# Optimization experiments

Hardware: AMD Instinct MI355X
Metric: run time of the kernel (lower is better)

Reference implementation:

```python
import jax, jax.numpy as jnp
import numpy as np

DIM = 512
MAX_LEN = 2048
SHARED = 128
EXPAND = 2 * DIM  # expansion_factor * dim
PROJ = 2 * EXPAND + SHARED
EPS = 1e-6
BATCH = 8


def _rope(x):
    # x: [n, d]; rotates last dim (split-half RoPE) with position along axis 0
    n, d = x.shape
    half = d // 2
    freq = jnp.arange(half, dtype=x.dtype) / float(half)
    inv_freq = 10000.0 ** (-freq)
    sinusoid = jnp.arange(n, dtype=x.dtype)[:, None] * inv_freq[None, :]  # [n, half]
    sin, cos = jnp.sin(sinusoid), jnp.cos(sinusoid)
    x1, x2 = x[:, :half], x[:, half:]
    return jnp.concatenate([x1 * cos - x2 * sin, x2 * cos + x1 * sin], axis=-1)


def _toeplitz_rope(n, a, b):
    # a, b: [max_len]; tile to [n, max_len], rope over positions, then outer product
    ar = _rope(jnp.tile(a[None, :], (n, 1)))
    br = _rope(jnp.tile(b[None, :], (n, 1)))
    return jnp.einsum('mk,nk->mn', ar, br)  # [n, n]


def setup_inputs() -> dict:
    key = jax.random.key(0)
    ks = jax.random.split(key, 8)
    std = 0.02
    return {
        'x': jax.random.normal(ks[0], (BATCH, MAX_LEN, DIM), jnp.float32),
        'W1': std * jax.random.normal(ks[1], (DIM, PROJ), jnp.float32),
        'b1': jnp.zeros((PROJ,), jnp.float32),
        'W2': std * jax.random.normal(ks[2], (EXPAND, DIM), jnp.float32),
        'b2': jnp.zeros((DIM,), jnp.float32),
        'rope_a': std * jax.random.normal(ks[3], (MAX_LEN,), jnp.float32),
        'rope_b': std * jax.random.normal(ks[4], (MAX_LEN,), jnp.float32),
        'gamma': std * jax.random.normal(ks[5], (2, SHARED), jnp.float32),
        'beta': jnp.zeros((2, SHARED), jnp.float32),
        'norm_scale': jnp.asarray(1.0, jnp.float32),
    }


def reference(x, W1, b1, W2, b2, rope_a, rope_b, gamma, beta, norm_scale):
    shortcut = x
    # ScaledNorm: x * rsqrt(mean(x^2)) * scale
    ms = jnp.mean(jnp.square(x), axis=-1, keepdims=True)
    xn = x * jax.lax.rsqrt(ms + EPS) * norm_scale
    # proj1 with swish activation
    uv = jax.nn.swish(xn @ W1 + b1)  # [b, n, PROJ]
    u = uv[..., :EXPAND]
    v = uv[..., EXPAND:2 * EXPAND]
    base = uv[..., 2 * EXPAND:]  # [b, n, SHARED]
    qk_base = base[:, :, None, :] * gamma + beta  # [b, n, 2, SHARED]
    q, k = qk_base[:, :, 0, :], qk_base[:, :, 1, :]
    qk = jnp.einsum('bnd,bmd->bnm', q, k) / float(MAX_LEN)
    qk = qk + _toeplitz_rope(MAX_LEN, rope_a, rope_b)
    kernel = jnp.square(jax.nn.relu(qk))  # sqrrelu
    o = u * jnp.einsum('bnm,bme->bne', kernel, v)
    return o @ W2 + b2 + shortcut
```

## Files before the change

### kernel.cpp

```cpp
#include <hip/hip_runtime.h>
#include <math.h>

#define SEQ    2048
#define DIMM   512
#define SH     128
#define EXP    1024
#define PROJ_  2176
#define NBATCH 8
#define ROWS   16384

#define KER_SCALE     16384.0f
#define KER_SCALE_INV (1.0f / 16384.0f)
#define QK_INV        (1.0f / (4096.0f * 2048.0f))
#define W8            64.0f
#define INV4096       (1.0f / 4096.0f)

typedef __attribute__((ext_vector_type(4))) float floatx4;
typedef __attribute__((ext_vector_type(8))) int   int8v;

__device__ __forceinline__ unsigned short f2bf(float f) {
  union { float f; unsigned int u; } v; v.f = f;
  unsigned int r = (v.u + 0x7fffu + ((v.u >> 16) & 1u)) >> 16;
  return (unsigned short)r;
}
__device__ __forceinline__ float bf2f(unsigned short h) {
  union { unsigned int u; float f; } v; v.u = ((unsigned int)h) << 16;
  return v.f;
}
__device__ __forceinline__ unsigned char f2fp8(float f) {
  return (unsigned char)(__builtin_amdgcn_cvt_pk_fp8_f32(f, 0.0f, 0, false) & 0xffu);
}
__device__ __forceinline__ unsigned int pk4fp8(float a, float b, float c, float d) {
  unsigned int w = __builtin_amdgcn_cvt_pk_fp8_f32(a, b, 0, false);
  return __builtin_amdgcn_cvt_pk_fp8_f32(c, d, w, true);
}
__device__ __forceinline__ float fp82f(unsigned char b) {
  int e = (b >> 3) & 15, m = b & 7;
  float v = ldexpf((float)(e ? (8 + m) : m), (e ? e : 1) - 10);
  return (b & 0x80) ? -v : v;
}

#if defined(__has_builtin)
#if __has_builtin(__builtin_amdgcn_cvt_f32_fp8)
#define HAVE_HW_FP8DEC 1
#endif
#endif
#ifdef HAVE_HW_FP8DEC
#define FP8DEC0(w) __builtin_amdgcn_cvt_f32_fp8((w), 0)
#define FP8DEC1(w) __builtin_amdgcn_cvt_f32_fp8((w), 1)
#define FP8DEC2(w) __builtin_amdgcn_cvt_f32_fp8((w), 2)
#define FP8DEC3(w) __builtin_amdgcn_cvt_f32_fp8((w), 3)
#else
#define FP8DEC0(w) fp82f((unsigned char)((w)))
#define FP8DEC1(w) fp82f((unsigned char)((w) >> 8))
#define FP8DEC2(w) fp82f((unsigned char)((w) >> 16))
#define FP8DEC3(w) fp82f((unsigned char)((w) >> 24))
#endif

__device__ __forceinline__ void async16(const void* g, void* l) {
  __builtin_amdgcn_global_load_lds(
      (const __attribute__((address_space(1))) void*)g,
      (__attribute__((address_space(3))) void*)l, 16, 0, 0);
}

__device__ __forceinline__ void transpose_tile_fp8(const float* __restrict__ in,
                                                   unsigned char* __restrict__ out,
                                                   int R, int C, int bx, int by, float* tile) {
  int tx = threadIdx.x & 31, ty = threadIdx.x >> 5;
  int c0 = bx * 32, r0 = by * 32;
  #pragma unroll
  for (int j = 0; j < 32; j += 8)
    tile[(ty + j) * 33 + tx] = in[(long)(r0 + ty + j) * C + c0 + tx];
  __syncthreads();
  #pragma unroll
  for (int j = 0; j < 32; j += 8)
    out[(long)(c0 + ty + j) * R + r0 + tx] = f2fp8(tile[tx * 33 + ty + j] * W8);
}

__global__ void prep_kernel(const float* __restrict__ x, const float* __restrict__ ns,
                            unsigned char* __restrict__ xq,
                            const float* __restrict__ W1, unsigned char* __restrict__ w1q,
                            const float* __restrict__ W2, unsigned char* __restrict__ w2q,
                            const float* __restrict__ ra, const float* __restrict__ rb,
                            float* __restrict__ tpl) {
  __shared__ float sh[33 * 32];
  const int b = blockIdx.x, tid = threadIdx.x;
  if (b < 4096) {
    int wave = tid >> 6, lane = tid & 63;
    long row = (long)b * 4 + wave;
    const float4* xr = (const float4*)(x + row * DIMM);
    float4 v0 = xr[lane], v1 = xr[lane + 64];
    float ss = v0.x*v0.x + v0.y*v0.y + v0.z*v0.z + v0.w*v0.w
             + v1.x*v1.x + v1.y*v1.y + v1.z*v1.z + v1.w*v1.w;
    #pragma unroll
    for (int o = 32; o > 0; o >>= 1) ss += __shfl_xor(ss, o);
    float sc = rsqrtf(ss * (1.0f / DIMM) + 1e-6f) * ns[0] * W8;
    uint2 pk;
    pk.x = pk4fp8(v0.x*sc, v0.y*sc, v0.z*sc, v0.w*sc);
    pk.y = pk4fp8(v1.x*sc, v1.y*sc, v1.z*sc, v1.w*sc);
    ((uint2*)(xq + row * DIMM))[lane] = pk;
  } else if (b < 6144) {
    const int d = b - 4096;
    float sc_ = 0.0f, ss_ = 0.0f;
    for (int k = tid; k < 1024; k += 256) {
      float a1 = ra[k], a2 = ra[k + 1024];
      float b1v = rb[k], b2v = rb[k + 1024];
      float p = a1 * b1v + a2 * b2v;
      float q = a1 * b2v - a2 * b1v;
      float th = exp2f((float)k * (-13.287712379549449f / 1024.0f));
      float ang = (float)d * th;
      sc_ += p * cosf(ang);
      ss_ += q * sinf(ang);
    }
    #pragma unroll
    for (int o = 32; o > 0; o >>= 1) {
      sc_ += __shfl_xor(sc_, o);
      ss_ += __shfl_xor(ss_, o);
    }
    int wave = tid >> 6, lane = tid & 63;
    if (lane == 0) { sh[wave] = sc_; sh[8 + wave] = ss_; }
    __syncthreads();
    if (tid == 0) {
      float Sc = sh[0] + sh[1] + sh[2] + sh[3];
      float Ss = sh[8] + sh[9] + sh[10] + sh[11];
      tpl[2047 + d] = Sc + Ss;
      if (d > 0) tpl[2047 - d] = Sc - Ss;
    }
  } else if (b < 7232) {
    int t = b - 6144;
    transpose_tile_fp8(W1, w1q, DIMM, PROJ_, t % 68, t / 68, sh);
  } else {
    int t = b - 7232;
    transpose_tile_fp8(W2, w2q, EXP, DIMM, t % 16, t / 16, sh);
  }
}

__device__ __forceinline__ void mfma_core_mx(const unsigned char* __restrict__ A,
                                             const unsigned char* __restrict__ B,
                                             int K, long rowBase, long colBase,
                                             unsigned char* smem, floatx4 acc[4][4]) {
  const int tid  = threadIdx.x;
  const int wave = tid >> 6;
  const int lane = tid & 63;
  const int wr   = (wave >> 1) * 64;
  const int wc   = (wave & 1) * 64;
  const int r_l  = lane >> 3;
  const int c8   = lane & 7;
  const int fm   = lane & 15;
  const int fq   = lane >> 4;

  floatx4 z = {0.0f, 0.0f, 0.0f, 0.0f};
  #pragma unroll
  for (int mi = 0; mi < 4; ++mi)
    #pragma unroll
    for (int ni = 0; ni < 4; ++ni) acc[mi][ni] = z;

  const unsigned char* aSrc[4];
  const unsigned char* bSrc[4];
  int ldsOff[4];
  #pragma unroll
  for (int j = 0; j < 4; ++j) {
    int row = j * 32 + wave * 8 + r_l;
    int g = c8 ^ (row & 7);
    aSrc[j] = A + (rowBase + row) * (long)K + g * 16;
    bSrc[j] = B + (colBase + row) * (long)K + g * 16;
    ldsOff[j] = (j * 32 + wave * 8) * 128;
  }

  union U8 { uint4 q[2]; int8v v; };
  const int nt = K >> 7;

  #pragma unroll
  for (int j = 0; j < 4; ++j) {
    async16(aSrc[j], smem + ldsOff[j]);
    async16(bSrc[j], smem + 16384 + ldsOff[j]);
  }
  if (nt > 1) {
    #pragma unroll
    for (int j = 0; j < 4; ++j) {
      async16(aSrc[j] + 128, smem + 32768 + ldsOff[j]);
      async16(bSrc[j] + 128, smem + 49152 + ldsOff[j]);
    }
  }

  int cur = 0;
  for (int t = 0; t < nt; ++t) {
    if (t + 1 < nt) {
      asm volatile("s_waitcnt vmcnt(8)" ::: "memory");
    } else {
      asm volatile("s_waitcnt vmcnt(0)" ::: "memory");
    }
    __builtin_amdgcn_s_barrier();
    __builtin_amdgcn_sched_barrier(0);

    const unsigned char* As = smem + cur * 32768;
    const unsigned char* Bs = As + 16384;
    int8v av[4], bv[4];
    #pragma unroll
    for (int mi = 0; mi < 4; ++mi) {
      int row = wr + mi * 16 + fm;
      int s0 = (2 * fq) ^ (row & 7);
      U8 u;
      u.q[0] = *(const uint4*)(As + row * 128 + s0 * 16);
      u.q[1] = *(const uint4*)(As + row * 128 + (s0 ^ 1) * 16);
      av[mi] = u.v;
    }
    #pragma unroll
    for (int ni = 0; ni < 4; ++ni) {
      int row = wc + ni * 16 + fm;
      int s0 = (2 * fq) ^ (row & 7);
      U8 u;
      u.q[0] = *(const uint4*)(Bs + row * 128 + s0 * 16);
      u.q[1] = *(const uint4*)(Bs + row * 128 + (s0 ^ 1) * 16);
      bv[ni] = u.v;
    }
    if (t + 2 < nt) {
      asm volatile("s_waitcnt lgkmcnt(0)" ::: "memory");
      __builtin_amdgcn_sched_barrier(0);
      __builtin_amdgcn_s_barrier();
      unsigned char* nb = smem + cur * 32768;
      int k0 = (t + 2) << 7;
      #pragma unroll
      for (int j = 0; j < 4; ++j) {
        async16(aSrc[j] + k0, nb + ldsOff[j]);
        async16(bSrc[j] + k0, nb + 16384 + ldsOff[j]);
      }
    }

    __builtin_amdgcn_s_setprio(1);
    #pragma unroll
    for (int mi = 0; mi < 4; ++mi)
      #pragma unroll
      for (int ni = 0; ni < 4; ++ni)
        acc[mi][ni] = __builtin_amdgcn_mfma_scale_f32_16x16x128_f8f6f4(
            av[mi], bv[ni], acc[mi][ni], 0, 0, 0, 0x7F7F7F7F, 0, 0x7F7F7F7F);
    __builtin_amdgcn_s_setprio(0);
    cur ^= 1;
  }
}

#define EPILOGUE_VARS                                         \
  const int lane = threadIdx.x & 63, wave = threadIdx.x >> 6; \
  const int wr = (wave >> 1) * 64, wc = (wave & 1) * 64;      \
  const int fr = (lane >> 4) * 4, fc = lane & 15;

__global__ void __launch_bounds__(256)
gemm_uv(const unsigned char* __restrict__ xq,
        const unsigned char* __restrict__ w1q,
        const float* __restrict__ b1,
        const float* __restrict__ gamma,
        const float* __restrict__ beta,
        unsigned char* __restrict__ uq,
        unsigned char* __restrict__ vT,
        unsigned char* __restrict__ qq,
        unsigned char* __restrict__ kq) {
  __shared__ __align__(16) unsigned char smem8[65536];
  floatx4 acc[4][4];
  long rowBase = (long)blockIdx.x * 128;
  long colBase = (long)blockIdx.y * 128;
  mfma_core_mx(xq, w1q, DIMM, rowBase, colBase, smem8, acc);
  EPILOGUE_VARS

  if (blockIdx.y < 8) {
    #pragma unroll
    for (int ni = 0; ni < 4; ++ni) {
      long col = colBase + wc + ni * 16 + fc;
      float bb = b1[col];
      #pragma unroll
      for (int mi = 0; mi < 4; ++mi)
      #pragma unroll
      for (int i = 0; i < 4; ++i) {
        long row = rowBase + wr + mi * 16 + fr + i;
        float t = acc[mi][ni][i] * INV4096 + bb;
        uq[row * EXP + col] = f2fp8(t / (1.0f + __expf(-t)) * W8);
      }
    }
  } else if (blockIdx.y < 16) {
    __syncthreads();
    #pragma unroll
    for (int ni = 0; ni < 4; ++ni) {
      int cl = wc + ni * 16 + fc;
      float bb = b1[colBase + cl];
      #pragma unroll
      for (int mi = 0; mi < 4; ++mi) {
        int rl = wr + mi * 16 + fr;
        float v[4];
        #pragma unroll
        for (int i = 0; i < 4; ++i) {
          float t = acc[mi][ni][i] * INV4096 + bb;
          v[i] = t / (1.0f + __expf(-t));
        }
        *(unsigned int*)(smem8 + cl * 136 + rl) = pk4fp8(v[0], v[1], v[2], v[3]);
      }
    }
    __syncthreads();
    long b_   = rowBase >> 11;
    long nblk = rowBase & 2047;
    long e0   = colBase - EXP;
    #pragma unroll
    for (int rep = 0; rep < 4; ++rep) {
      int cl = rep * 32 + (threadIdx.x >> 3);
      int n0 = (threadIdx.x & 7) * 16;
      uint4 v16 = *(const uint4*)(smem8 + cl * 136 + n0);
      *(uint4*)(vT + (b_ * EXP + e0 + cl) * (long)SEQ + nblk + n0) = v16;
    }
  } else {
    #pragma unroll
    for (int ni = 0; ni < 4; ++ni) {
      long col = colBase + wc + ni * 16 + fc;
      int dd = (int)(col - 2 * EXP);
      float bb = b1[col];
      float g0 = gamma[dd], g1 = gamma[SH + dd];
      float be0 = beta[dd], be1 = beta[SH + dd];
      #pragma unroll
      for (int mi = 0; mi < 4; ++mi)
      #pragma unroll
      for (int i = 0; i < 4; ++i) {
        long row = rowBase + wr + mi * 16 + fr + i;
        float t = acc[mi][ni][i] * INV4096 + bb;
        float s = t / (1.0f + __expf(-t));
        qq[row * SH + dd] = f2fp8((s * g0 + be0) * W8);
        kq[row * SH + dd] = f2fp8((s * g1 + be1) * W8);
      }
    }
  }
}

__global__ void __launch_bounds__(256)
gemm_qk(const unsigned char* __restrict__ kq,
        const unsigned char* __restrict__ qq,
        const float* __restrict__ tpl,
        unsigned char* __restrict__ ker) {
  __shared__ __align__(16) unsigned char smem8[33792];
  float* tplS = (float*)(smem8 + 32768);
  floatx4 acc[4][4];
  int L = blockIdx.x;
  long b = L & 7;
  int w = L >> 3;
  long mBase = (long)(w & 15) * 128;
  long nBase = (long)(w >> 4) * 128;
  long D = nBase - mBase;
  if (threadIdx.x < 64)
    ((float4*)tplS)[threadIdx.x] = *(const float4*)(tpl + D + 1920 + 4 * (long)threadIdx.x);
  mfma_core_mx(kq + b * SEQ * SH, qq + b * SEQ * SH, SH, mBase, nBase, smem8, acc);
  unsigned char* kerb = ker + b * (long)SEQ * SEQ;
  EPILOGUE_VARS
  (void)fr;
  __syncthreads();
  #pragma unroll
  for (int mi = 0; mi < 4; ++mi)
  #pragma unroll
  for (int ni = 0; ni < 4; ++ni) {
    int m_loc0 = wr + mi * 16 + (lane >> 4) * 4;
    int n_loc  = wc + ni * 16 + fc;
    float v[4];
    #pragma unroll
    for (int i = 0; i < 4; ++i) {
      float val = acc[mi][ni][i] * QK_INV + tplS[n_loc - m_loc0 - i + 127];
      float r = fmaxf(val, 0.0f);
      v[i] = fminf(r * r * KER_SCALE, 440.0f);
    }
    *(unsigned int*)(smem8 + n_loc * 136 + m_loc0) = pk4fp8(v[0], v[1], v[2], v[3]);
  }
  __syncthreads();
  #pragma unroll
  for (int rep = 0; rep < 4; ++rep) {
    int n_loc = rep * 32 + (threadIdx.x >> 3);
    int m_seg = (threadIdx.x & 7) * 16;
    uint4 v16 = *(const uint4*)(smem8 + n_loc * 136 + m_seg);
    *(uint4*)(kerb + (nBase + n_loc) * (long)SEQ + mBase + m_seg) = v16;
  }
}

__global__ void __launch_bounds__(256)
gemm_pv(const unsigned char* __restrict__ ker,
        const unsigned char* __restrict__ vT,
        const unsigned char* __restrict__ uq,
        unsigned char* __restrict__ obq) {
  __shared__ __align__(16) unsigned char smem8[65536];
  floatx4 acc[4][4];
  int L = blockIdx.x;
  long b = L & 7;
  int w = L >> 3;
  long eBase = (long)(w & 7) * 128;
  long nBase = (long)(w >> 3) * 128;
  mfma_core_mx(vT + b * (long)EXP * SEQ, ker + b * (long)SEQ * SEQ, SEQ,
               eBase, nBase, smem8, acc);
  const unsigned char* ub = uq + b * (long)SEQ * EXP;
  unsigned char* obb = obq + b * (long)SEQ * EXP;
  EPILOGUE_VARS
  (void)fr;
  __syncthreads();
  #pragma unroll
  for (int mi = 0; mi < 4; ++mi)
  #pragma unroll
  for (int ni = 0; ni < 4; ++ni) {
    int e_loc0 = wr + mi * 16 + (lane >> 4) * 4;
    int n_loc  = wc + ni * 16 + fc;
    unsigned int uw = *(const unsigned int*)(ub + (nBase + n_loc) * (long)EXP + eBase + e_loc0);
    float u0 = FP8DEC0(uw), u1 = FP8DEC1(uw), u2 = FP8DEC2(uw), u3 = FP8DEC3(uw);
    float v0 = acc[mi][ni][0] * KER_SCALE_INV * u0;
    float v1 = acc[mi][ni][1] * KER_SCALE_INV * u1;
    float v2 = acc[mi][ni][2] * KER_SCALE_INV * u2;
    float v3 = acc[mi][ni][3] * KER_SCALE_INV * u3;
    *(unsigned int*)(smem8 + n_loc * 136 + e_loc0) = pk4fp8(v0, v1, v2, v3);
  }
  __syncthreads();
  #pragma unroll
  for (int rep = 0; rep < 4; ++rep) {
    int n_loc = rep * 32 + (threadIdx.x >> 3);
    int e_seg = (threadIdx.x & 7) * 16;
    uint4 v16 = *(const uint4*)(smem8 + n_loc * 136 + e_seg);
    *(uint4*)(obb + (nBase + n_loc) * (long)EXP + eBase + e_seg) = v16;
  }
}

__global__ void __launch_bounds__(256)
gemm_out(const unsigned char* __restrict__ obq,
         const unsigned char* __restrict__ w2q,
         const float* __restrict__ b2,
         const float* __restrict__ x,
         float* __restrict__ out) {
  __shared__ __align__(16) unsigned char smem8[65536];
  floatx4 acc[4][4];
  long rowBase = (long)blockIdx.x * 128;
  long colBase = (long)blockIdx.y * 128;
  mfma_core_mx(obq, w2q, EXP, rowBase, colBase, smem8, acc);
  EPILOGUE_VARS
  #pragma unroll
  for (int mi = 0; mi < 4; ++mi)
  #pragma unroll
  for (int ni = 0; ni < 4; ++ni)
  #pragma unroll
  for (int i = 0; i < 4; ++i) {
    long row = rowBase + wr + mi * 16 + fr + i;
    long col = colBase + wc + ni * 16 + fc;
    out[row * DIMM + col] = acc[mi][ni][i] * INV4096 + b2[col] + x[row * DIMM + col];
  }
}

extern "C" void kernel_launch(void* const* d_in, const int* in_sizes, int n_in,
                              void* d_out, int out_size, void* d_ws, size_t ws_size,
                              hipStream_t stream) {
  const float* x          = (const float*)d_in[0];
  const float* W1         = (const float*)d_in[1];
  const float* b1         = (const float*)d_in[2];
  const float* W2         = (const float*)d_in[3];
  const float* b2         = (const float*)d_in[4];
  const float* rope_a     = (const float*)d_in[5];
  const float* rope_b     = (const float*)d_in[6];
  const float* gamma      = (const float*)d_in[7];
  const float* beta       = (const float*)d_in[8];
  const float* norm_scale = (const float*)d_in[9];
  float* out = (float*)d_out;

  char* ws = (char*)d_ws;
  size_t off = 0;
  auto nxt = [&](size_t bytes) -> void* {
    void* p = ws + off;
    off += (bytes + 255) & ~(size_t)255;
    return p;
  };
  unsigned char*  xq  = (unsigned char*)nxt((size_t)ROWS * DIMM);
  unsigned char*  w1q = (unsigned char*)nxt((size_t)PROJ_ * DIMM);
  unsigned char*  w2q = (unsigned char*)nxt((size_t)DIMM * EXP);
  unsigned char*  uq  = (unsigned char*)nxt((size_t)ROWS * EXP);
  unsigned char*  vT  = (unsigned char*)nxt((size_t)NBATCH * EXP * SEQ);
  unsigned char*  qq  = (unsigned char*)nxt((size_t)ROWS * SH);
  unsigned char*  kq  = (unsigned char*)nxt((size_t)ROWS * SH);
  float*          tpl = (float*)nxt((size_t)4096 * 4);
  unsigned char*  ker = (unsigned char*)nxt((size_t)NBATCH * SEQ * SEQ);
  unsigned char*  obq = (unsigned char*)nxt((size_t)ROWS * EXP);

  prep_kernel<<<7744, 256, 0, stream>>>(x, norm_scale, xq, W1, w1q, W2, w2q,
                                        rope_a, rope_b, tpl);
  gemm_uv<<<dim3(ROWS / 128, PROJ_ / 128), 256, 0, stream>>>(xq, w1q, b1, gamma, beta,
                                                             uq, vT, qq, kq);
  gemm_qk<<<2048, 256, 0, stream>>>(kq, qq, tpl, ker);
  gemm_pv<<<1024, 256, 0, stream>>>(ker, vT, uq, obq);
  gemm_out<<<dim3(ROWS / 128, DIMM / 128), 256, 0, stream>>>(obq, w2q, b2, x, out);
}
```

Measured before the change: 209.9 us.

## Recompute u projection inside PV GEMM instead of materializing uq

```diff
diff --git a/kernel.cpp b/kernel.cpp
--- a/kernel.cpp
+++ b/kernel.cpp
@@ -39,23 +39,6 @@
   float v = ldexpf((float)(e ? (8 + m) : m), (e ? e : 1) - 10);
   return (b & 0x80) ? -v : v;
 }
-
-#if defined(__has_builtin)
-#if __has_builtin(__builtin_amdgcn_cvt_f32_fp8)
-#define HAVE_HW_FP8DEC 1
-#endif
-#endif
-#ifdef HAVE_HW_FP8DEC
-#define FP8DEC0(w) __builtin_amdgcn_cvt_f32_fp8((w), 0)
-#define FP8DEC1(w) __builtin_amdgcn_cvt_f32_fp8((w), 1)
-#define FP8DEC2(w) __builtin_amdgcn_cvt_f32_fp8((w), 2)
-#define FP8DEC3(w) __builtin_amdgcn_cvt_f32_fp8((w), 3)
-#else
-#define FP8DEC0(w) fp82f((unsigned char)((w)))
-#define FP8DEC1(w) fp82f((unsigned char)((w) >> 8))
-#define FP8DEC2(w) fp82f((unsigned char)((w) >> 16))
-#define FP8DEC3(w) fp82f((unsigned char)((w) >> 24))
-#endif
 
 __device__ __forceinline__ void async16(const void* g, void* l) {
   __builtin_amdgcn_global_load_lds(
@@ -250,32 +233,17 @@
         const float* __restrict__ b1,
         const float* __restrict__ gamma,
         const float* __restrict__ beta,
-        unsigned char* __restrict__ uq,
         unsigned char* __restrict__ vT,
         unsigned char* __restrict__ qq,
         unsigned char* __restrict__ kq) {
   __shared__ __align__(16) unsigned char smem8[65536];
   floatx4 acc[4][4];
   long rowBase = (long)blockIdx.x * 128;
-  long colBase = (long)blockIdx.y * 128;
+  long colBase = (long)(blockIdx.y + 8) * 128;
   mfma_core_mx(xq, w1q, DIMM, rowBase, colBase, smem8, acc);
   EPILOGUE_VARS
 
   if (blockIdx.y < 8) {
-    #pragma unroll
-    for (int ni = 0; ni < 4; ++ni) {
-      long col = colBase + wc + ni * 16 + fc;
-      float bb = b1[col];
-      #pragma unroll
-      for (int mi = 0; mi < 4; ++mi)
-      #pragma unroll
-      for (int i = 0; i < 4; ++i) {
-        long row = rowBase + wr + mi * 16 + fr + i;
-        float t = acc[mi][ni][i] * INV4096 + bb;
-        uq[row * EXP + col] = f2fp8(t / (1.0f + __expf(-t)) * W8);
-      }
-    }
-  } else if (blockIdx.y < 16) {
     __syncthreads();
     #pragma unroll
     for (int ni = 0; ni < 4; ++ni) {
@@ -375,35 +343,38 @@
 __global__ void __launch_bounds__(256)
 gemm_pv(const unsigned char* __restrict__ ker,
         const unsigned char* __restrict__ vT,
-        const unsigned char* __restrict__ uq,
+        const unsigned char* __restrict__ xq,
+        const unsigned char* __restrict__ w1q,
+        const float* __restrict__ b1,
         unsigned char* __restrict__ obq) {
   __shared__ __align__(16) unsigned char smem8[65536];
-  floatx4 acc[4][4];
+  floatx4 accU[4][4], accP[4][4];
   int L = blockIdx.x;
   long b = L & 7;
   int w = L >> 3;
   long eBase = (long)(w & 7) * 128;
   long nBase = (long)(w >> 3) * 128;
+  mfma_core_mx(w1q, xq + b * (long)SEQ * DIMM, DIMM, eBase, nBase, smem8, accU);
+  __syncthreads();
   mfma_core_mx(vT + b * (long)EXP * SEQ, ker + b * (long)SEQ * SEQ, SEQ,
-               eBase, nBase, smem8, acc);
-  const unsigned char* ub = uq + b * (long)SEQ * EXP;
+               eBase, nBase, smem8, accP);
   unsigned char* obb = obq + b * (long)SEQ * EXP;
   EPILOGUE_VARS
-  (void)fr;
   __syncthreads();
   #pragma unroll
   for (int mi = 0; mi < 4; ++mi)
   #pragma unroll
   for (int ni = 0; ni < 4; ++ni) {
-    int e_loc0 = wr + mi * 16 + (lane >> 4) * 4;
+    int e_loc0 = wr + mi * 16 + fr;
     int n_loc  = wc + ni * 16 + fc;
-    unsigned int uw = *(const unsigned int*)(ub + (nBase + n_loc) * (long)EXP + eBase + e_loc0);
-    float u0 = FP8DEC0(uw), u1 = FP8DEC1(uw), u2 = FP8DEC2(uw), u3 = FP8DEC3(uw);
-    float v0 = acc[mi][ni][0] * KER_SCALE_INV * u0;
-    float v1 = acc[mi][ni][1] * KER_SCALE_INV * u1;
-    float v2 = acc[mi][ni][2] * KER_SCALE_INV * u2;
-    float v3 = acc[mi][ni][3] * KER_SCALE_INV * u3;
-    *(unsigned int*)(smem8 + n_loc * 136 + e_loc0) = pk4fp8(v0, v1, v2, v3);
+    float v[4];
+    #pragma unroll
+    for (int i = 0; i < 4; ++i) {
+      float t = accU[mi][ni][i] * INV4096 + b1[eBase + e_loc0 + i];
+      float s = t / (1.0f + __expf(-t)) * W8;
+      v[i] = accP[mi][ni][i] * KER_SCALE_INV * s;
+    }
+    *(unsigned int*)(smem8 + n_loc * 136 + e_loc0) = pk4fp8(v[0], v[1], v[2], v[3]);
   }
   __syncthreads();
   #pragma unroll
@@ -464,7 +435,6 @@
   unsigned char*  xq  = (unsigned char*)nxt((size_t)ROWS * DIMM);
   unsigned char*  w1q = (unsigned char*)nxt((size_t)PROJ_ * DIMM);
   unsigned char*  w2q = (unsigned char*)nxt((size_t)DIMM * EXP);
-  unsigned char*  uq  = (unsigned char*)nxt((size_t)ROWS * EXP);
   unsigned char*  vT  = (unsigned char*)nxt((size_t)NBATCH * EXP * SEQ);
   unsigned char*  qq  = (unsigned char*)nxt((size_t)ROWS * SH);
   unsigned char*  kq  = (unsigned char*)nxt((size_t)ROWS * SH);
@@ -474,9 +444,9 @@
 
   prep_kernel<<<7744, 256, 0, stream>>>(x, norm_scale, xq, W1, w1q, W2, w2q,
                                         rope_a, rope_b, tpl);
-  gemm_uv<<<dim3(ROWS / 128, PROJ_ / 128), 256, 0, stream>>>(xq, w1q, b1, gamma, beta,
-                                                             uq, vT, qq, kq);
+  gemm_uv<<<dim3(ROWS / 128, 9), 256, 0, stream>>>(xq, w1q, b1, gamma, beta,
+                                                   vT, qq, kq);
   gemm_qk<<<2048, 256, 0, stream>>>(kq, qq, tpl, ker);
-  gemm_pv<<<1024, 256, 0, stream>>>(ker, vT, uq, obq);
+  gemm_pv<<<1024, 256, 0, stream>>>(ker, vT, xq, w1q, b1, obq);
   gemm_out<<<dim3(ROWS / 128, DIMM / 128), 256, 0, stream>>>(obq, w2q, b2, x, out);
 }
```

Result: slower. 228.4 us (+8.8%).
